# Kernel optimization log

Hardware: AMD Instinct MI355X
Metric: run time of the kernel (lower is better)

The kernel has to match this reference:

```python
import jax, jax.numpy as jnp
import numpy as np

NUM_GRAPHS = 256  # fixed number of segments (batch.max()+1 in the torch code)

def setup_inputs() -> dict:
    key = jax.random.key(0)
    k1, k2, k3, k4, k5 = jax.random.split(key, 5)
    N, D, H = 200000, 256, 128
    x = jax.random.normal(k1, (N, D), dtype=jnp.float32)
    batch = jnp.sort(jax.random.randint(k2, (N,), 0, NUM_GRAPHS)).astype(jnp.int64)
    # attention MLP params: Linear(D->H), Tanh, Linear(H->1)
    w1 = jax.random.normal(k3, (D, H), dtype=jnp.float32) / np.sqrt(D)
    b1 = jnp.zeros((H,), dtype=jnp.float32)
    w2 = jax.random.normal(k4, (H, 1), dtype=jnp.float32) / np.sqrt(H)
    b2 = jnp.zeros((1,), dtype=jnp.float32)
    return {"x": x, "batch": batch, "w1": w1, "b1": b1, "w2": w2, "b2": b2}

def reference(x, batch, w1, b1, w2, b2):
    # attention scores: Linear -> tanh -> Linear -> [N,1]
    scores = jnp.tanh(x @ w1 + b1) @ w2 + b2          # [N,1]
    # NOTE: faithful to the original: softmax over ALL nodes (dim=0), not per-graph
    attn = jax.nn.softmax(scores, axis=0)              # [N,1]
    weighted = x * attn                                # [N,D]
    # masked per-graph sum == segment sum over graph ids
    out = jax.ops.segment_sum(weighted, batch, num_segments=NUM_GRAPHS)  # [B,D]
    return out
```

## Files before the change

### kernel.cpp

```cpp
#include <hip/hip_runtime.h>

#define NGRAPHS 256
#define DIM     256
#define HID     128
#define TILE    128

typedef __attribute__((ext_vector_type(8))) short bf16x8;
typedef __attribute__((ext_vector_type(4))) float f32x4;

__device__ __forceinline__ ushort f2bf_rne(float f) {
    unsigned u = __float_as_uint(f);
    unsigned r = u + 0x7fffu + ((u >> 16) & 1u);
    return (ushort)(r >> 16);
}
__device__ __forceinline__ float bf2f(ushort h) {
    return __uint_as_float(((unsigned)h) << 16);
}
__device__ __forceinline__ float tanh_fast(float x) {
    float e = __expf(2.0f * x);
    return 1.0f - 2.0f * __builtin_amdgcn_rcpf(1.0f + e);
}

__device__ __forceinline__ void glds16(const void* g, void* l) {
    __builtin_amdgcn_global_load_lds(
        (const __attribute__((address_space(1))) unsigned int*)g,
        (__attribute__((address_space(3))) unsigned int*)l, 16, 0, 0);
}

__device__ __forceinline__ void cvt8(float4 v0, float4 v1, bf16x8& h, bf16x8& l) {
    float f[8] = {v0.x, v0.y, v0.z, v0.w, v1.x, v1.y, v1.z, v1.w};
    unsigned hu[8], lu[8];
#pragma unroll
    for (int i = 0; i < 8; ++i) {
        unsigned u = __float_as_uint(f[i]);
        unsigned hb = u & 0xffff0000u;
        hu[i] = u;
        lu[i] = __float_as_uint(f[i] - __uint_as_float(hb));
    }
    union { unsigned w[4]; bf16x8 v; } H, L;
#pragma unroll
    for (int j = 0; j < 4; ++j) {
        H.w[j] = (hu[2 * j] >> 16) | (hu[2 * j + 1] & 0xffff0000u);
        L.w[j] = (lu[2 * j] >> 16) | (lu[2 * j + 1] & 0xffff0000u);
    }
    h = H.v; l = L.v;
}

__global__ void k_prep(const float* __restrict__ w1, ushort* __restrict__ w1f)
{
    int idx = blockIdx.x * 256 + threadIdx.x;
    int k  = idx >> 7, nn = idx & 127;
    int ks = k >> 5, lhi = (k >> 3) & 3, j = k & 7;
    int nf = nn >> 4, llo = nn & 15;
    int lane = lhi * 16 + llo;
    float v = w1[idx];
    ushort hb = f2bf_rne(v);
    ushort lb = f2bf_rne(v - bf2f(hb));
    int base = (ks * 8 + nf) * 1024 + lane * 8 + j;
    w1f[base]       = hb;
    w1f[base + 512] = lb;
}

__global__ __launch_bounds__(256, 3) void k_scores(
    const float* __restrict__ x, const int* __restrict__ batch,
    const ushort* __restrict__ w1f,
    const float* __restrict__ b1, const float* __restrict__ w2,
    const float* __restrict__ b2,
    float* __restrict__ wsp, float* __restrict__ wse, int* __restrict__ wsid,
    int n)
{
    __shared__ float  xs[TILE * 32];
    __shared__ ushort bs[8 * 1024];
    __shared__ float  evals[TILE];
    __shared__ int    gid[TILE];
    __shared__ float  sred[4][2][DIM];
    __shared__ float  ep[4];

    const int t    = threadIdx.x;
    const int b    = blockIdx.x;
    const int r0   = b * TILE;
    const int wid  = t >> 6;
    const int lane = t & 63;
    const int lhi  = lane >> 4;
    const int llo  = lane & 15;

    if (t < TILE) {
        int r = r0 + t;
        gid[t] = batch[r < n ? r : (n - 1)];
    }

    f32x4 acc[2][8];
#pragma unroll
    for (int i = 0; i < 2; ++i)
#pragma unroll
        for (int j = 0; j < 8; ++j) acc[i][j] = (f32x4){0.f, 0.f, 0.f, 0.f};

    const int ra0 = wid * 32 + llo;
    const int ra1 = ra0 + 16;
    const int rb7 = ra0 & 7;
    const int c00 = (ra0 * 8 + ((2 * lhi)     ^ rb7)) * 4;
    const int c01 = (ra0 * 8 + ((2 * lhi + 1) ^ rb7)) * 4;
    const int c10 = (ra1 * 8 + ((2 * lhi)     ^ rb7)) * 4;
    const int c11 = (ra1 * 8 + ((2 * lhi + 1) ^ rb7)) * 4;

    for (int ks = 0; ks < 8; ++ks) {
#pragma unroll
        for (int i = 0; i < 4; ++i) {
            int p = i * 256 + t;
            int r = p >> 3, s = p & 7;
            int q = s ^ (r & 7);
            int rsrc = r0 + r; if (rsrc >= n) rsrc = n - 1;
            glds16(x + (size_t)rsrc * DIM + ks * 32 + q * 4,
                   &xs[(i * 256 + wid * 64) * 4]);
            glds16(w1f + (size_t)ks * 8192 + (size_t)p * 8,
                   &bs[(i * 256 + wid * 64) * 8]);
        }
        __syncthreads();

        float4 a0 = *(const float4*)&xs[c00];
        float4 a1 = *(const float4*)&xs[c01];
        float4 c0 = *(const float4*)&xs[c10];
        float4 c1 = *(const float4*)&xs[c11];
        bf16x8 ah0, al0, ah1, al1;
        cvt8(a0, a1, ah0, al0);
        cvt8(c0, c1, ah1, al1);

#pragma unroll
        for (int nf = 0; nf < 8; ++nf) {
            bf16x8 bh = *(const bf16x8*)&bs[(nf * 2 + 0) * 512 + lane * 8];
            bf16x8 bl = *(const bf16x8*)&bs[(nf * 2 + 1) * 512 + lane * 8];
            acc[0][nf] = __builtin_amdgcn_mfma_f32_16x16x32_bf16(ah0, bh, acc[0][nf], 0, 0, 0);
            acc[1][nf] = __builtin_amdgcn_mfma_f32_16x16x32_bf16(ah1, bh, acc[1][nf], 0, 0, 0);
            acc[0][nf] = __builtin_amdgcn_mfma_f32_16x16x32_bf16(ah0, bl, acc[0][nf], 0, 0, 0);
            acc[1][nf] = __builtin_amdgcn_mfma_f32_16x16x32_bf16(ah1, bl, acc[1][nf], 0, 0, 0);
            acc[0][nf] = __builtin_amdgcn_mfma_f32_16x16x32_bf16(al0, bh, acc[0][nf], 0, 0, 0);
            acc[1][nf] = __builtin_amdgcn_mfma_f32_16x16x32_bf16(al1, bh, acc[1][nf], 0, 0, 0);
        }
        __syncthreads();
    }

    float b2v = b2[0];
    float b1v[8], w2v[8];
#pragma unroll
    for (int nf = 0; nf < 8; ++nf) {
        b1v[nf] = b1[nf * 16 + llo];
        w2v[nf] = w2[nf * 16 + llo];
    }
    float sc[8];
#pragma unroll
    for (int mf = 0; mf < 2; ++mf)
#pragma unroll
        for (int rg = 0; rg < 4; ++rg) {
            float p = 0.f;
#pragma unroll
            for (int nf = 0; nf < 8; ++nf)
                p += tanh_fast(acc[mf][nf][rg] + b1v[nf]) * w2v[nf];
            sc[mf * 4 + rg] = p;
        }
#pragma unroll
    for (int off = 1; off < 16; off <<= 1)
#pragma unroll
        for (int q = 0; q < 8; ++q) sc[q] += __shfl_xor(sc[q], off, 64);

    if (llo == 0) {
#pragma unroll
        for (int mf = 0; mf < 2; ++mf)
#pragma unroll
            for (int rg = 0; rg < 4; ++rg) {
                int row = wid * 32 + mf * 16 + lhi * 4 + rg;
                float s = sc[mf * 4 + rg] + b2v;
                evals[row] = (r0 + row < n) ? __expf(s) : 0.f;
            }
    }
    __syncthreads();

    {
        const int g0 = gid[0];
        float4 a0 = {0.f, 0.f, 0.f, 0.f}, a1 = {0.f, 0.f, 0.f, 0.f};
        for (int bt = 0; bt < 4; ++bt) {
            float4 xv[8];
#pragma unroll
            for (int j = 0; j < 8; ++j) {
                int rsrc = r0 + wid * 32 + bt * 8 + j;
                if (rsrc >= n) rsrc = n - 1;
                xv[j] = *(const float4*)(x + (size_t)rsrc * DIM + lane * 4);
            }
#pragma unroll
            for (int j = 0; j < 8; ++j) {
                int row = wid * 32 + bt * 8 + j;
                float e = evals[row];
                if (gid[row] != g0) {
                    a1.x = fmaf(e, xv[j].x, a1.x); a1.y = fmaf(e, xv[j].y, a1.y);
                    a1.z = fmaf(e, xv[j].z, a1.z); a1.w = fmaf(e, xv[j].w, a1.w);
                } else {
                    a0.x = fmaf(e, xv[j].x, a0.x); a0.y = fmaf(e, xv[j].y, a0.y);
                    a0.z = fmaf(e, xv[j].z, a0.z); a0.w = fmaf(e, xv[j].w, a0.w);
                }
            }
        }
        *(float4*)&sred[wid][0][lane * 4] = a0;
        *(float4*)&sred[wid][1][lane * 4] = a1;
    }
    __syncthreads();
    {
        float s0 = sred[0][0][t] + sred[1][0][t] + sred[2][0][t] + sred[3][0][t];
        float s1 = sred[0][1][t] + sred[1][1][t] + sred[2][1][t] + sred[3][1][t];
        wsp[(size_t)b * 512 + t]       = s0;
        wsp[(size_t)b * 512 + 256 + t] = s1;
        if (t == 0) wsid[b] = gid[0];
    }

    float rsum = (t < TILE) ? evals[t] : 0.f;
#pragma unroll
    for (int off = 32; off; off >>= 1) rsum += __shfl_down(rsum, off, 64);
    if ((t & 63) == 0) ep[t >> 6] = rsum;
    __syncthreads();
    if (t == 0) wse[b] = ep[0] + ep[1];
}

__global__ __launch_bounds__(256) void k_combine(
    const int* __restrict__ batch, const float* __restrict__ wsp,
    const float* __restrict__ wse, const int* __restrict__ wsid,
    float* __restrict__ out, int n, int nblk)
{
    __shared__ float sred[256];
    __shared__ int bounds[2];
    const int g = blockIdx.x;
    const int d = threadIdx.x;

    float p = 0.f;
    for (int i = d; i < nblk; i += 256) p += wse[i];
    sred[d] = p;
    __syncthreads();
    for (int s = 128; s; s >>= 1) {
        if (d < s) sred[d] += sred[d + s];
        __syncthreads();
    }
    const float S = sred[0];

    if (d < 2) {
        int v = g + d;
        int lo = 0, hi = n;
        while (lo < hi) { int mid = (lo + hi) >> 1; if (batch[mid] < v) lo = mid + 1; else hi = mid; }
        bounds[d] = lo;
    }
    __syncthreads();

    const int st = bounds[0], en = bounds[1];
    float acc = 0.f;
    if (st < en) {
        for (int bb = st >> 7; bb <= (en - 1) >> 7; ++bb) {
            int slot = (wsid[bb] == g) ? 0 : 1;
            acc += wsp[(size_t)bb * 512 + slot * 256 + d];
        }
    }
    out[g * 256 + d] = acc / S;
}

extern "C" void kernel_launch(void* const* d_in, const int* in_sizes, int n_in,
                              void* d_out, int out_size, void* d_ws, size_t ws_size,
                              hipStream_t stream)
{
    const float* x     = (const float*)d_in[0];
    const int*   batch = (const int*)d_in[1];
    const float* w1    = (const float*)d_in[2];
    const float* b1    = (const float*)d_in[3];
    const float* w2    = (const float*)d_in[4];
    const float* b2    = (const float*)d_in[5];
    float* out = (float*)d_out;

    const int n    = in_sizes[1];
    const int nblk = (n + TILE - 1) / TILE;

    ushort* w1f = (ushort*)d_ws;
    float*  wsp = (float*)((char*)d_ws + (size_t)DIM * HID * 2 * sizeof(ushort));
    float*  wse = wsp + (size_t)nblk * 512;
    int*    wsid = (int*)(wse + nblk);

    k_prep<<<dim3(DIM * HID / 256), dim3(256), 0, stream>>>(w1, w1f);
    k_scores<<<dim3(nblk), dim3(256), 0, stream>>>(x, batch, w1f,
                                                   b1, w2, b2, wsp, wse, wsid, n);
    k_combine<<<dim3(NGRAPHS), dim3(256), 0, stream>>>(batch, wsp, wse, wsid,
                                                       out, n, nblk);
}
```

Before: 94.78 us.

## Double-buffer LDS staging of x and W1 tiles in score kernel

Splits the shared-memory tiles for x and the pre-split W1 fragments into two buffers. The next K-slice is loaded with async global-to-LDS copies while MFMA runs on the current slice, and one barrier per iteration is removed. Load addresses are hoisted out of the loop, and the reduction scratch area is aliased onto the same shared block. The larger LDS footprint lowers the launch-bounds occupancy hint from 3 to 2 blocks per CU, which may cut latency hiding on what is largely a bandwidth-bound read of x.

```diff
diff --git a/kernel.cpp b/kernel.cpp
--- a/kernel.cpp
+++ b/kernel.cpp
@@ -61,7 +61,7 @@
     w1f[base + 512] = lb;
 }
 
-__global__ __launch_bounds__(256, 3) void k_scores(
+__global__ __launch_bounds__(256, 2) void k_scores(
     const float* __restrict__ x, const int* __restrict__ batch,
     const ushort* __restrict__ w1f,
     const float* __restrict__ b1, const float* __restrict__ w2,
@@ -69,12 +69,13 @@
     float* __restrict__ wsp, float* __restrict__ wse, int* __restrict__ wsid,
     int n)
 {
-    __shared__ float  xs[TILE * 32];
-    __shared__ ushort bs[8 * 1024];
-    __shared__ float  evals[TILE];
-    __shared__ int    gid[TILE];
-    __shared__ float  sred[4][2][DIM];
-    __shared__ float  ep[4];
+    __shared__ __align__(16) unsigned char smem[65536];
+    float  (*xs)[TILE * 32] = (float(*)[TILE * 32])smem;
+    ushort (*bs)[8 * 1024]  = (ushort(*)[8 * 1024])(smem + 32768);
+    float  (*sred)[2][DIM]  = (float(*)[2][DIM])smem;
+    __shared__ float evals[TILE];
+    __shared__ int   gid[TILE];
+    __shared__ float ep[4];
 
     const int t    = threadIdx.x;
     const int b    = blockIdx.x;
@@ -89,6 +90,28 @@
         gid[t] = batch[r < n ? r : (n - 1)];
     }
 
+    size_t xoff[4], boff[4];
+    int    xl[4], bl[4];
+#pragma unroll
+    for (int i = 0; i < 4; ++i) {
+        int p = i * 256 + t;
+        int r = p >> 3, s = p & 7;
+        int q = s ^ (r & 7);
+        int rsrc = r0 + r; if (rsrc >= n) rsrc = n - 1;
+        xoff[i] = (size_t)rsrc * DIM + q * 4;
+        boff[i] = (size_t)p * 8;
+        xl[i]   = (i * 256 + wid * 64) * 4;
+        bl[i]   = (i * 256 + wid * 64) * 8;
+    }
+
+#define STAGE(sel, KS) do {                                          \
+    _Pragma("unroll")                                                \
+    for (int i = 0; i < 4; ++i) {                                    \
+        glds16(x + xoff[i] + (KS) * 32, &xs[sel][xl[i]]);            \
+        glds16(w1f + (size_t)(KS) * 8192 + boff[i], &bs[sel][bl[i]]);\
+    }                                                                \
+} while (0)
+
     f32x4 acc[2][8];
 #pragma unroll
     for (int i = 0; i < 2; ++i)
@@ -103,32 +126,25 @@
     const int c10 = (ra1 * 8 + ((2 * lhi)     ^ rb7)) * 4;
     const int c11 = (ra1 * 8 + ((2 * lhi + 1) ^ rb7)) * 4;
 
+    STAGE(0, 0);
+    __syncthreads();
+#pragma unroll
     for (int ks = 0; ks < 8; ++ks) {
-#pragma unroll
-        for (int i = 0; i < 4; ++i) {
-            int p = i * 256 + t;
-            int r = p >> 3, s = p & 7;
-            int q = s ^ (r & 7);
-            int rsrc = r0 + r; if (rsrc >= n) rsrc = n - 1;
-            glds16(x + (size_t)rsrc * DIM + ks * 32 + q * 4,
-                   &xs[(i * 256 + wid * 64) * 4]);
-            glds16(w1f + (size_t)ks * 8192 + (size_t)p * 8,
-                   &bs[(i * 256 + wid * 64) * 8]);
-        }
-        __syncthreads();
-
-        float4 a0 = *(const float4*)&xs[c00];
-        float4 a1 = *(const float4*)&xs[c01];
-        float4 c0 = *(const float4*)&xs[c10];
-        float4 c1 = *(const float4*)&xs[c11];
+        const int cur = ks & 1;
+        if (ks < 7) STAGE(cur ^ 1, ks + 1);
+
+        float4 a0 = *(const float4*)&xs[cur][c00];
+        float4 a1 = *(const float4*)&xs[cur][c01];
+        float4 c0 = *(const float4*)&xs[cur][c10];
+        float4 c1 = *(const float4*)&xs[cur][c11];
         bf16x8 ah0, al0, ah1, al1;
         cvt8(a0, a1, ah0, al0);
         cvt8(c0, c1, ah1, al1);
 
 #pragma unroll
         for (int nf = 0; nf < 8; ++nf) {
-            bf16x8 bh = *(const bf16x8*)&bs[(nf * 2 + 0) * 512 + lane * 8];
-            bf16x8 bl = *(const bf16x8*)&bs[(nf * 2 + 1) * 512 + lane * 8];
+            bf16x8 bh = *(const bf16x8*)&bs[cur][(nf * 2 + 0) * 512 + lane * 8];
+            bf16x8 bl = *(const bf16x8*)&bs[cur][(nf * 2 + 1) * 512 + lane * 8];
             acc[0][nf] = __builtin_amdgcn_mfma_f32_16x16x32_bf16(ah0, bh, acc[0][nf], 0, 0, 0);
             acc[1][nf] = __builtin_amdgcn_mfma_f32_16x16x32_bf16(ah1, bh, acc[1][nf], 0, 0, 0);
             acc[0][nf] = __builtin_amdgcn_mfma_f32_16x16x32_bf16(ah0, bl, acc[0][nf], 0, 0, 0);
@@ -138,6 +154,7 @@
         }
         __syncthreads();
     }
+#undef STAGE
 
     float b2v = b2[0];
     float b1v[8], w2v[8];
```

Measured after the change: 96.04 us. About the same (+1.3%).
